# Kernel tuning notes

Measured on AMD Instinct MI355X. Metric: run time of the kernel, lower is better.

The kernel has to match this reference:

```python
import jax, jax.numpy as jnp
import numpy as np

N_E = 8192
E_DIM = 256
N_TOK = 32768
MU = 0.25  # commitment weight; beta=0 so diversity loss is skipped


def setup_inputs() -> dict:
    key = jax.random.key(0)
    k1, k2, k3 = jax.random.split(key, 3)
    x = jax.random.normal(k1, (N_TOK, E_DIM), dtype=jnp.float32)
    # codebook init: uniform(-1/n_e, 1/n_e) as in the torch module
    emb = jax.random.uniform(k2, (N_E, E_DIM), dtype=jnp.float32,
                             minval=-1.0 / N_E, maxval=1.0 / N_E)
    label = jax.random.randint(k3, (N_TOK,), 0, 10, dtype=jnp.int32)
    return {"x": x, "emb": emb, "label": label, "idx": 0}


def reference(x, emb, label, idx):
    # latent: [N, e_dim]
    latent = x.reshape(-1, emb.shape[1])
    # pairwise squared distances via norm + matmul: [N, n_e]
    d = (jnp.sum(latent * latent, axis=1, keepdims=True)
         + jnp.sum(emb * emb, axis=1)[None, :]
         - 2.0 * (latent @ emb.T))
    indices = jnp.argmin(d, axis=-1)                 # [N]
    x_q = emb[indices].reshape(x.shape)              # gather
    commitment_loss = jnp.mean(jnp.square(jax.lax.stop_gradient(x_q) - x))
    codebook_loss = jnp.mean(jnp.square(x_q - jax.lax.stop_gradient(x)))
    loss = codebook_loss + MU * commitment_loss      # beta=0 -> no diversity term
    x_q_out = x + jax.lax.stop_gradient(x_q - x)     # straight-through estimator
    return x_q_out, loss, indices.reshape(x.shape[:-1])
```

## Files before the change

### kernel.cpp

```cpp
#include <hip/hip_runtime.h>
#include <float.h>
#include <stdint.h>

#define N_TOK 32768
#define N_E   8192
#define EDIM  256
#define MU_W  0.25f
#define NSPLIT 4
#define NRANGE 2048
#define BMr 64
#define MARGIN_F 4096.0f
#define OFFSETF (-0x1p21f)
#define XSCALE 512.0f
#define ESCALE -131072.0f

typedef _Float16 f16;
typedef _Float16 f16x8 __attribute__((ext_vector_type(8)));
typedef _Float16 f16x4 __attribute__((ext_vector_type(4)));
typedef float f32x4 __attribute__((ext_vector_type(4)));
typedef unsigned int u32;
typedef unsigned long long u64;

#define WS_EMB16   0
#define WS_SX      4194304
#define WS_SE      4325376
#define WS_SE25    4358144
#define WS_CAND    4390912
#define WS_PART    6488064
#define WS_RCNT    6619136
#define WS_RLIST   6619392
#define WS_RBEST   6750464

__device__ inline void gload_lds16(const void* g, void* l) {
  __builtin_amdgcn_global_load_lds(
      (const __attribute__((address_space(1))) unsigned int*)g,
      (__attribute__((address_space(3))) unsigned int*)l, 16, 0, 0);
}

__device__ inline u32 umax_(u32 a, u32 b) { return a > b ? a : b; }
__device__ inline u32 umin_(u32 a, u32 b) { return a < b ? a : b; }

__device__ inline u32 med3u(u32 a, u32 b, u32 c) {
  u32 r;
  asm("v_med3_u32 %0, %1, %2, %3" : "=v"(r) : "v"(a), "v"(b), "v"(c));
  return r;
}

__device__ inline void ins4max(u32 v, u32& a, u32& b, u32& c, u32& d) {
  u32 na = umax_(a, v);
  u32 nb = med3u(a, b, v);
  u32 nc = med3u(b, c, v);
  u32 nd = med3u(c, d, v);
  a = na; b = nb; c = nc; d = nd;
}

__global__ __launch_bounds__(256) void conv_fused(const float* __restrict__ emb,
                                                  const float* __restrict__ x,
                                                  char* __restrict__ dst16,
                                                  float* __restrict__ se,
                                                  float* __restrict__ se25,
                                                  float* __restrict__ sx,
                                                  u32* __restrict__ rcnt) {
  if (blockIdx.x == 0 && threadIdx.x == 0) rcnt[0] = 0u;
  int wave = threadIdx.x >> 6;
  int lane = threadIdx.x & 63;
  int row = blockIdx.x * 4 + wave;
  if (row < N_E) {
    const float4 v = *(const float4*)(emb + (size_t)row * EDIM + lane * 4);
    float s = (v.x * v.x + v.y * v.y) + (v.z * v.z + v.w * v.w);
#pragma unroll
    for (int off = 32; off >= 1; off >>= 1) s += __shfl_xor(s, off);
    if (lane == 0) { se[row] = s; se25[row] = s * 0x1p25f; }
    f16x4 h;
    h[0] = (f16)(v.x * ESCALE); h[1] = (f16)(v.y * ESCALE);
    h[2] = (f16)(v.z * ESCALE); h[3] = (f16)(v.w * ESCALE);
    *(f16x4*)(dst16 + (size_t)(row >> 4) * 8192 + (lane >> 1) * 256 +
              (row & 15) * 16 + (lane & 1) * 8) = h;
  } else {
    int xr = row - N_E;
    const float4 v = *(const float4*)(x + (size_t)xr * EDIM + lane * 4);
    float s = (v.x * v.x + v.y * v.y) + (v.z * v.z + v.w * v.w);
#pragma unroll
    for (int off = 32; off >= 1; off >>= 1) s += __shfl_xor(s, off);
    if (lane == 0) sx[xr] = s;
  }
}

__global__ __launch_bounds__(256, 2) void vq_main(const float* __restrict__ x,
                                                  const char* __restrict__ e16,
                                                  const float* __restrict__ se25,
                                                  u32* __restrict__ cand) {
  __shared__ __align__(16) char lds[81920];
  char* Abuf = lds;
  char* Bbuf = lds + 32768;

  const int tid = threadIdx.x;
  const int lane = tid & 63;
  const int wn = tid >> 6;
  const int l15 = lane & 15;
  const int lg  = lane >> 4;
  const int split = blockIdx.x & 3;
  const int bm = (blockIdx.x >> 2) * BMr;
  const int nbase = split * NRANGE;
  const int splitRB = split * 128;

  int aOff[4], bOff[4];
#pragma unroll
  for (int mi = 0; mi < 4; ++mi) aOff[mi] = mi * 8192 + lg * 256 + l15 * 16;
#pragma unroll
  for (int ni = 0; ni < 4; ++ni) bOff[ni] = (wn * 4 + ni) * 1024 + lg * 256 + l15 * 16;

  int svo[4], sdo[4];
#pragma unroll
  for (int l = 0; l < 4; ++l) {
    int u = l * 256 + tid;
    svo[l] = (u >> 6) * 8192 + (u & 63) * 16;
    sdo[l] = (u >> 6) * 1024 + (u & 63) * 16;
  }

  {
    const int row = tid >> 2, seg = tid & 3;
    const float4* xs = (const float4*)(x + (size_t)(bm + row) * EDIM + seg * 64);
    const int ab = (row >> 4) * 8192 + (row & 15) * 16;
#pragma unroll
    for (int u = 0; u < 8; ++u) {
      float4 a0 = xs[2 * u], a1 = xs[2 * u + 1];
      f16x8 hv;
      hv[0] = (f16)(a0.x * XSCALE); hv[1] = (f16)(a0.y * XSCALE);
      hv[2] = (f16)(a0.z * XSCALE); hv[3] = (f16)(a0.w * XSCALE);
      hv[4] = (f16)(a1.x * XSCALE); hv[5] = (f16)(a1.y * XSCALE);
      hv[6] = (f16)(a1.z * XSCALE); hv[7] = (f16)(a1.w * XSCALE);
      *(f16x8*)&Abuf[ab + (seg * 8 + u) * 256] = hv;
    }
  }
  {
    const size_t eb = (size_t)splitRB * 8192;
#pragma unroll
    for (int l = 0; l < 4; ++l) gload_lds16(e16 + eb + svo[l], Bbuf + sdo[l]);
  }
  __syncthreads();

  u32 d1[16], d2[16], d3[16], d4[16];
#pragma unroll
  for (int s = 0; s < 16; ++s) { d1[s] = 0u; d2[s] = 0u; d3[s] = 0u; d4[s] = 0u; }

  const int idl = wn * 64 + l15;

  int bufc = 0;
  for (int t = 0; t < 8; ++t) {
    float sev[4];
#pragma unroll
    for (int ni = 0; ni < 4; ++ni)
      sev[ni] = se25[nbase + t * 256 + wn * 64 + ni * 16 + l15];

    f32x4 acc[4][4];
#pragma unroll
    for (int mi = 0; mi < 4; ++mi)
#pragma unroll
      for (int ni = 0; ni < 4; ++ni)
        acc[mi][ni] = (f32x4){OFFSETF, OFFSETF, OFFSETF, OFFSETF};

#pragma unroll
    for (int q = 0; q < 8; ++q) {
      const int c = t * 8 + q;
      const int cn = (c + 1) & 63;
      const int tn = cn >> 3, qn = cn & 7;
      const int bufn = (bufc == 2) ? 0 : bufc + 1;
      {
        const size_t ebN = (size_t)(splitRB + tn * 16) * 8192 + qn * 1024;
        char* dstN = Bbuf + bufn * 16384;
#pragma unroll
        for (int l = 0; l < 4; ++l) gload_lds16(e16 + ebN + svo[l], dstN + sdo[l]);
      }
      asm volatile("s_waitcnt vmcnt(4)" ::: "memory");
      __builtin_amdgcn_s_barrier();
      __builtin_amdgcn_sched_barrier(0);
      {
        const char* Bc = Bbuf + bufc * 16384;
        f16x8 av[4], bv[4];
#pragma unroll
        for (int mi = 0; mi < 4; ++mi) av[mi] = *(const f16x8*)&Abuf[aOff[mi] + q * 1024];
#pragma unroll
        for (int ni = 0; ni < 4; ++ni) bv[ni] = *(const f16x8*)&Bc[bOff[ni]];
        __builtin_amdgcn_s_setprio(1);
#pragma unroll
        for (int mi = 0; mi < 4; ++mi)
#pragma unroll
          for (int ni = 0; ni < 4; ++ni)
            acc[mi][ni] = __builtin_amdgcn_mfma_f32_16x16x32_f16(av[mi], bv[ni], acc[mi][ni], 0, 0, 0);
        __builtin_amdgcn_s_setprio(0);
      }
      bufc = bufn;
    }

#pragma unroll
    for (int ni = 0; ni < 4; ++ni) {
      const u32 id = (u32)(t * 256 + ni * 16 + idl);
#pragma unroll
      for (int mi = 0; mi < 4; ++mi)
#pragma unroll
        for (int r = 0; r < 4; ++r) {
          u32 up = (__float_as_uint(acc[mi][ni][r] + sev[ni]) & 0xFFFFF800u) | id;
          int s = mi * 4 + r;
          ins4max(up, d1[s], d2[s], d3[s], d4[s]);
        }
    }
  }

  __syncthreads();

#pragma unroll
  for (int off = 8; off >= 1; off >>= 1) {
#pragma unroll
    for (int s = 0; s < 16; ++s) {
      u32 e1 = (u32)__shfl_xor((int)d1[s], off);
      u32 e2 = (u32)__shfl_xor((int)d2[s], off);
      u32 e3 = (u32)__shfl_xor((int)d3[s], off);
      u32 e4 = (u32)__shfl_xor((int)d4[s], off);
      ins4max(e1, d1[s], d2[s], d3[s], d4[s]);
      ins4max(e2, d1[s], d2[s], d3[s], d4[s]);
      ins4max(e3, d1[s], d2[s], d3[s], d4[s]);
      ins4max(e4, d1[s], d2[s], d3[s], d4[s]);
    }
  }
  u32 (*scratch)[4][16][4] = (u32 (*)[4][16][4])lds;
  if (l15 == 0) {
#pragma unroll
    for (int s = 0; s < 16; ++s) {
      scratch[wn][lg][s][0] = d1[s];
      scratch[wn][lg][s][1] = d2[s];
      scratch[wn][lg][s][2] = d3[s];
      scratch[wn][lg][s][3] = d4[s];
    }
  }
  __syncthreads();
  if (tid < 64) {
    const int row = tid;
    const int mi = row >> 4, lgr = (row >> 2) & 3, rr = row & 3;
    const int s = mi * 4 + rr;
    u32 a1 = scratch[0][lgr][s][0];
    u32 a2 = scratch[0][lgr][s][1];
    u32 a3 = scratch[0][lgr][s][2];
    u32 a4 = scratch[0][lgr][s][3];
#pragma unroll
    for (int w = 1; w < 4; ++w) {
#pragma unroll
      for (int c = 0; c < 4; ++c)
        ins4max(scratch[w][lgr][s][c], a1, a2, a3, a4);
    }
    size_t base = (size_t)split * (N_TOK * 4) + (size_t)(bm + row) * 4;
    cand[base + 0] = a1; cand[base + 1] = a2; cand[base + 2] = a3; cand[base + 3] = a4;
  }
}

__global__ __launch_bounds__(256) void vq_gather_kernel(
    const float* __restrict__ x, const float* __restrict__ emb,
    const float* __restrict__ sx, const float* __restrict__ se,
    const u32* __restrict__ cand,
    float* __restrict__ out_q, float* __restrict__ out_idx,
    float* __restrict__ partials,
    u32* __restrict__ rcnt, u32* __restrict__ rlist, u64* __restrict__ rbest) {
  const int token = blockIdx.x;
  const int tid = threadIdx.x;
  __shared__ int s_j;
  __shared__ int s_cnt;
  __shared__ int s_cj[16];
  __shared__ float s_dv[16];
  __shared__ float red[4];

  if (tid == 0) {
    u32 u[16];
    float uf[16];
    float gmin = FLT_MAX;
#pragma unroll
    for (int sp = 0; sp < 4; ++sp)
#pragma unroll
      for (int c = 0; c < 4; ++c) {
        u32 v = cand[(size_t)sp * (N_TOK * 4) + (size_t)token * 4 + c];
        u[sp * 4 + c] = v;
        float f = __uint_as_float(v);
        uf[sp * 4 + c] = f;
        gmin = fminf(gmin, f);
      }
    bool guard = false;
#pragma unroll
    for (int sp = 0; sp < 4; ++sp) guard = guard || (uf[sp * 4 + 3] <= gmin + MARGIN_F);
    int cnt;
    if (guard) {
      u32 slot = atomicAdd(rcnt, 1u);
      rlist[slot] = (u32)token;
      rbest[slot] = ~0ull;
      cnt = -1;
    } else {
      cnt = 0;
#pragma unroll
      for (int sp = 0; sp < 4; ++sp)
#pragma unroll
        for (int c = 0; c < 4; ++c) {
          int k = sp * 4 + c;
          if (uf[k] <= gmin + MARGIN_F)
            s_cj[cnt++] = sp * NRANGE + (int)(u[k] & 0x7FFu);
        }
      if (cnt == 1) s_j = s_cj[0];
    }
    s_cnt = cnt;
  }
  __syncthreads();
  int cnt = s_cnt;
  if (cnt < 0) return;
  if (cnt > 1 && tid < cnt) {
    int j = s_cj[tid];
    const float* xr = x + (size_t)token * EDIM;
    const float* er = emb + (size_t)j * EDIM;
    float a = 0.f;
    for (int k = 0; k < EDIM; ++k) a = fmaf(xr[k], er[k], a);
    s_dv[tid] = (sx[token] + se[j]) - 2.0f * a;
  }
  __syncthreads();
  if (cnt > 1 && tid == 0) {
    float bd = s_dv[0]; int bj = s_cj[0];
    for (int c = 1; c < cnt; ++c) {
      float d = s_dv[c]; int j = s_cj[c];
      if (d < bd || (d == bd && j < bj)) { bd = d; bj = j; }
    }
    s_j = bj;
  }
  __syncthreads();
  const int j = s_j;
  if (tid == 0) out_idx[token] = (float)j;
  float xv = x[(size_t)token * EDIM + tid];
  float q  = emb[(size_t)j * EDIM + tid];
  float diff = q - xv;
  out_q[(size_t)token * EDIM + tid] = xv + diff;
  float sq = diff * diff;
#pragma unroll
  for (int off = 32; off >= 1; off >>= 1) sq += __shfl_xor(sq, off);
  const int wave = tid >> 6, lane = tid & 63;
  if (lane == 0) red[wave] = sq;
  __syncthreads();
  if (tid == 0) partials[token] = (red[0] + red[1]) + (red[2] + red[3]);
}

__global__ __launch_bounds__(256) void vq_rescan_scan(
    const float* __restrict__ x, const float* __restrict__ emb,
    const float* __restrict__ sx, const float* __restrict__ se,
    const u32* __restrict__ rcnt, const u32* __restrict__ rlist,
    u64* __restrict__ rbest) {
  const int tid = threadIdx.x;
  const int n = (int)rcnt[0];
  const int total = n * 32;
  __shared__ float xs[EDIM];
  __shared__ u64 rw[4];

  for (int w = blockIdx.x; w < total; w += gridDim.x) {
    const int it = w >> 5, chunk = w & 31;
    const int token = (int)rlist[it];
    __syncthreads();
    xs[tid] = x[(size_t)token * EDIM + tid];
    __syncthreads();
    const float sxt = sx[token];
    const int j = chunk * 256 + tid;
    const float* er = emb + (size_t)j * EDIM;
    float a = 0.f;
#pragma unroll 8
    for (int k4 = 0; k4 < 64; ++k4) {
      float4 e4 = ((const float4*)er)[k4];
      float4 x4 = ((const float4*)xs)[k4];
      a = fmaf(x4.x, e4.x, a);
      a = fmaf(x4.y, e4.y, a);
      a = fmaf(x4.z, e4.z, a);
      a = fmaf(x4.w, e4.w, a);
    }
    float d = (sxt + se[j]) - 2.0f * a;
    u64 pk = ((u64)__float_as_uint(d) << 32) | (u32)j;
    const int lane = tid & 63, wave = tid >> 6;
#pragma unroll
    for (int off = 32; off >= 1; off >>= 1) {
      u64 o = __shfl_xor(pk, off);
      pk = o < pk ? o : pk;
    }
    if (lane == 0) rw[wave] = pk;
    __syncthreads();
    if (tid == 0) {
      u64 b = rw[0];
#pragma unroll
      for (int ww = 1; ww < 4; ++ww) b = rw[ww] < b ? rw[ww] : b;
      atomicMin(rbest + it, b);
    }
  }
}

__global__ __launch_bounds__(256) void vq_rescan_write(
    const float* __restrict__ x, const float* __restrict__ emb,
    const u32* __restrict__ rcnt, const u32* __restrict__ rlist,
    const u64* __restrict__ rbest,
    float* __restrict__ out_q, float* __restrict__ out_idx,
    float* __restrict__ partials) {
  const int tid = threadIdx.x;
  const int n = (int)rcnt[0];
  __shared__ float red[4];

  for (int it = blockIdx.x; it < n; it += gridDim.x) {
    const int token = (int)rlist[it];
    const int j = (int)(u32)(rbest[it] & 0xFFFFFFFFull);
    if (tid == 0) out_idx[token] = (float)j;
    float xv = x[(size_t)token * EDIM + tid];
    float q  = emb[(size_t)j * EDIM + tid];
    float diff = q - xv;
    out_q[(size_t)token * EDIM + tid] = xv + diff;
    float sq = diff * diff;
#pragma unroll
    for (int off = 32; off >= 1; off >>= 1) sq += __shfl_xor(sq, off);
    const int lane = tid & 63, wave = tid >> 6;
    __syncthreads();
    if (lane == 0) red[wave] = sq;
    __syncthreads();
    if (tid == 0) partials[token] = (red[0] + red[1]) + (red[2] + red[3]);
  }
}

__global__ __launch_bounds__(256) void vq_loss_kernel(const float* __restrict__ partials,
                                                      float* __restrict__ loss_out) {
  const int tid = threadIdx.x;
  float s = 0.f;
  for (int i = tid; i < N_TOK; i += 256) s += partials[i];
  __shared__ float red[4];
#pragma unroll
  for (int off = 32; off >= 1; off >>= 1) s += __shfl_xor(s, off);
  const int wave = tid >> 6, lane = tid & 63;
  if (lane == 0) red[wave] = s;
  __syncthreads();
  if (tid == 0) {
    float tot = (red[0] + red[1]) + (red[2] + red[3]);
    float mean = tot / (float)(N_TOK * EDIM);
    loss_out[0] = mean + MU_W * mean;
  }
}

extern "C" void kernel_launch(void* const* d_in, const int* in_sizes, int n_in,
                              void* d_out, int out_size, void* d_ws, size_t ws_size,
                              hipStream_t stream) {
  const float* x   = (const float*)d_in[0];
  const float* emb = (const float*)d_in[1];

  float* out      = (float*)d_out;
  float* out_q    = out;
  float* out_loss = out + (size_t)N_TOK * EDIM;
  float* out_idx  = out_loss + 1;

  char* w = (char*)d_ws;
  char*  emb16    = w + WS_EMB16;
  float* sx       = (float*)(w + WS_SX);
  float* se       = (float*)(w + WS_SE);
  float* se25     = (float*)(w + WS_SE25);
  u32*   cand     = (u32*)(w + WS_CAND);
  float* partials = (float*)(w + WS_PART);
  u32*   rcnt     = (u32*)(w + WS_RCNT);
  u32*   rlist    = (u32*)(w + WS_RLIST);
  u64*   rbest    = (u64*)(w + WS_RBEST);

  conv_fused<<<(N_E + N_TOK) / 4, 256, 0, stream>>>(emb, x, emb16, se, se25, sx, rcnt);

  vq_main<<<NSPLIT * (N_TOK / BMr), 256, 0, stream>>>(x, emb16, se25, cand);

  vq_gather_kernel<<<N_TOK, 256, 0, stream>>>(x, emb, sx, se, cand, out_q, out_idx, partials,
                                              rcnt, rlist, rbest);
  vq_rescan_scan<<<2048, 256, 0, stream>>>(x, emb, sx, se, rcnt, rlist, rbest);
  vq_rescan_write<<<64, 256, 0, stream>>>(x, emb, rcnt, rlist, rbest, out_q, out_idx, partials);
  vq_loss_kernel<<<1, 256, 0, stream>>>(partials, out_loss);
}
```

Before: 314.8 us.

## Switch candidate search GEMM from fp16 to int8 MFMA with 8-way codebook split

Result: slower. 968.6 us (+207.7%).

```diff
diff --git a/kernel.cpp b/kernel.cpp
--- a/kernel.cpp
+++ b/kernel.cpp
@@ -6,26 +6,21 @@
 #define N_E   8192
 #define EDIM  256
 #define MU_W  0.25f
-#define NSPLIT 4
-#define NRANGE 2048
+#define NSPLIT 8
+#define NRANGE 1024
 #define BMr 64
-#define MARGIN_F 4096.0f
-#define OFFSETF (-0x1p21f)
-#define XSCALE 512.0f
-#define ESCALE -131072.0f
-
-typedef _Float16 f16;
-typedef _Float16 f16x8 __attribute__((ext_vector_type(8)));
-typedef _Float16 f16x4 __attribute__((ext_vector_type(4)));
-typedef float f32x4 __attribute__((ext_vector_type(4)));
+#define MARGIN_I 6144u
+#define SEVB_BIAS (1 << 20)
+
+typedef int i32x4 __attribute__((ext_vector_type(4)));
 typedef unsigned int u32;
 typedef unsigned long long u64;
 
-#define WS_EMB16   0
-#define WS_SX      4194304
-#define WS_SE      4325376
-#define WS_SE25    4358144
-#define WS_CAND    4390912
+#define WS_E8      0
+#define WS_SX      2097152
+#define WS_SE      2228224
+#define WS_SEVB    2260992
+#define WS_CAND    2293760
 #define WS_PART    6488064
 #define WS_RCNT    6619136
 #define WS_RLIST   6619392
@@ -37,7 +32,6 @@
       (__attribute__((address_space(3))) unsigned int*)l, 16, 0, 0);
 }
 
-__device__ inline u32 umax_(u32 a, u32 b) { return a > b ? a : b; }
 __device__ inline u32 umin_(u32 a, u32 b) { return a < b ? a : b; }
 
 __device__ inline u32 med3u(u32 a, u32 b, u32 c) {
@@ -46,19 +40,21 @@
   return r;
 }
 
-__device__ inline void ins4max(u32 v, u32& a, u32& b, u32& c, u32& d) {
-  u32 na = umax_(a, v);
+__device__ inline void ins4min(u32 v, u32& a, u32& b, u32& c, u32& d) {
+  u32 na = umin_(a, v);
   u32 nb = med3u(a, b, v);
   u32 nc = med3u(b, c, v);
   u32 nd = med3u(c, d, v);
   a = na; b = nb; c = nc; d = nd;
 }
 
+__device__ inline int clamp127(int q) { return q < -127 ? -127 : (q > 127 ? 127 : q); }
+
 __global__ __launch_bounds__(256) void conv_fused(const float* __restrict__ emb,
                                                   const float* __restrict__ x,
-                                                  char* __restrict__ dst16,
+                                                  char* __restrict__ e8,
                                                   float* __restrict__ se,
-                                                  float* __restrict__ se25,
+                                                  int* __restrict__ sevb,
                                                   float* __restrict__ sx,
                                                   u32* __restrict__ rcnt) {
   if (blockIdx.x == 0 && threadIdx.x == 0) rcnt[0] = 0u;
@@ -70,12 +66,19 @@
     float s = (v.x * v.x + v.y * v.y) + (v.z * v.z + v.w * v.w);
 #pragma unroll
     for (int off = 32; off >= 1; off >>= 1) s += __shfl_xor(s, off);
-    if (lane == 0) { se[row] = s; se25[row] = s * 0x1p25f; }
-    f16x4 h;
-    h[0] = (f16)(v.x * ESCALE); h[1] = (f16)(v.y * ESCALE);
-    h[2] = (f16)(v.z * ESCALE); h[3] = (f16)(v.w * ESCALE);
-    *(f16x4*)(dst16 + (size_t)(row >> 4) * 8192 + (lane >> 1) * 256 +
-              (row & 15) * 16 + (lane & 1) * 8) = h;
+    if (lane == 0) se[row] = s;
+    int q0 = (int)rintf(v.x * 524288.f);
+    int q1 = (int)rintf(v.y * 524288.f);
+    int q2 = (int)rintf(v.z * 524288.f);
+    int q3 = (int)rintf(v.w * 524288.f);
+    int s2 = q0 * q0 + q1 * q1 + q2 * q2 + q3 * q3;
+#pragma unroll
+    for (int off = 32; off >= 1; off >>= 1) s2 += __shfl_xor(s2, off);
+    if (lane == 0) sevb[row] = ((s2 + 16384) >> 15) + SEVB_BIAS;
+    u32 w = (u32)(q0 & 255) | ((u32)(q1 & 255) << 8) |
+            ((u32)(q2 & 255) << 16) | ((u32)(q3 & 255) << 24);
+    *(u32*)(e8 + (size_t)(row >> 4) * 4096 + (lane >> 2) * 256 +
+            (row & 15) * 16 + (lane & 3) * 4) = w;
   } else {
     int xr = row - N_E;
     const float4 v = *(const float4*)(x + (size_t)xr * EDIM + lane * 4);
@@ -87,26 +90,25 @@
 }
 
 __global__ __launch_bounds__(256, 2) void vq_main(const float* __restrict__ x,
-                                                  const char* __restrict__ e16,
-                                                  const float* __restrict__ se25,
+                                                  const char* __restrict__ e8,
+                                                  const int* __restrict__ sevb,
                                                   u32* __restrict__ cand) {
-  __shared__ __align__(16) char lds[81920];
-  char* Abuf = lds;
-  char* Bbuf = lds + 32768;
+  __shared__ __align__(16) char lds[65536];
+  char* Bbuf = lds + 16384;
 
   const int tid = threadIdx.x;
   const int lane = tid & 63;
   const int wn = tid >> 6;
   const int l15 = lane & 15;
   const int lg  = lane >> 4;
-  const int split = blockIdx.x & 3;
-  const int bm = (blockIdx.x >> 2) * BMr;
+  const int split = blockIdx.x & 7;
+  const int bm = (blockIdx.x >> 3) * BMr;
   const int nbase = split * NRANGE;
-  const int splitRB = split * 128;
+  const int splitRB = split * 64;
 
   int aOff[4], bOff[4];
 #pragma unroll
-  for (int mi = 0; mi < 4; ++mi) aOff[mi] = mi * 8192 + lg * 256 + l15 * 16;
+  for (int mi = 0; mi < 4; ++mi) aOff[mi] = mi * 4096 + lg * 256 + l15 * 16;
 #pragma unroll
   for (int ni = 0; ni < 4; ++ni) bOff[ni] = (wn * 4 + ni) * 1024 + lg * 256 + l15 * 16;
 
@@ -114,95 +116,101 @@
 #pragma unroll
   for (int l = 0; l < 4; ++l) {
     int u = l * 256 + tid;
-    svo[l] = (u >> 6) * 8192 + (u & 63) * 16;
-    sdo[l] = (u >> 6) * 1024 + (u & 63) * 16;
-  }
+    svo[l] = (u >> 6) * 4096 + (u & 63) * 16;
+    sdo[l] = u * 16;
+  }
+
+  int sv[4][4];
+#pragma unroll
+  for (int ct = 0; ct < 4; ++ct)
+#pragma unroll
+    for (int ni = 0; ni < 4; ++ni)
+      sv[ct][ni] = sevb[nbase + ct * 256 + wn * 64 + ni * 16 + l15];
 
   {
     const int row = tid >> 2, seg = tid & 3;
     const float4* xs = (const float4*)(x + (size_t)(bm + row) * EDIM + seg * 64);
-    const int ab = (row >> 4) * 8192 + (row & 15) * 16;
-#pragma unroll
-    for (int u = 0; u < 8; ++u) {
-      float4 a0 = xs[2 * u], a1 = xs[2 * u + 1];
-      f16x8 hv;
-      hv[0] = (f16)(a0.x * XSCALE); hv[1] = (f16)(a0.y * XSCALE);
-      hv[2] = (f16)(a0.z * XSCALE); hv[3] = (f16)(a0.w * XSCALE);
-      hv[4] = (f16)(a1.x * XSCALE); hv[5] = (f16)(a1.y * XSCALE);
-      hv[6] = (f16)(a1.z * XSCALE); hv[7] = (f16)(a1.w * XSCALE);
-      *(f16x8*)&Abuf[ab + (seg * 8 + u) * 256] = hv;
-    }
-  }
-  {
-    const size_t eb = (size_t)splitRB * 8192;
-#pragma unroll
-    for (int l = 0; l < 4; ++l) gload_lds16(e16 + eb + svo[l], Bbuf + sdo[l]);
-  }
-  __syncthreads();
+    char* ab = lds + (row >> 4) * 4096 + (row & 15) * 16;
+#pragma unroll
+    for (int u = 0; u < 4; ++u) {
+      u32 w[4];
+#pragma unroll
+      for (int p = 0; p < 4; ++p) {
+        float4 f = xs[u * 4 + p];
+        int q0 = clamp127((int)rintf(f.x * 16.f));
+        int q1 = clamp127((int)rintf(f.y * 16.f));
+        int q2 = clamp127((int)rintf(f.z * 16.f));
+        int q3 = clamp127((int)rintf(f.w * 16.f));
+        w[p] = (u32)(q0 & 255) | ((u32)(q1 & 255) << 8) |
+               ((u32)(q2 & 255) << 16) | ((u32)(q3 & 255) << 24);
+      }
+      *(uint4*)(ab + (seg * 4 + u) * 256) = make_uint4(w[0], w[1], w[2], w[3]);
+    }
+  }
+  __syncthreads();
+
+#pragma unroll
+  for (int c0 = 0; c0 < 2; ++c0) {
+    const char* src = e8 + (size_t)(splitRB + (c0 >> 2) * 16) * 4096 + (c0 & 3) * 1024;
+    char* dst = Bbuf + (c0 % 3) * 16384;
+#pragma unroll
+    for (int l = 0; l < 4; ++l) gload_lds16(src + svo[l], dst + sdo[l]);
+  }
 
   u32 d1[16], d2[16], d3[16], d4[16];
 #pragma unroll
-  for (int s = 0; s < 16; ++s) { d1[s] = 0u; d2[s] = 0u; d3[s] = 0u; d4[s] = 0u; }
+  for (int s = 0; s < 16; ++s) { d1[s] = 0xFFFFFFFFu; d2[s] = 0xFFFFFFFFu; d3[s] = 0xFFFFFFFFu; d4[s] = 0xFFFFFFFFu; }
 
   const int idl = wn * 64 + l15;
 
-  int bufc = 0;
-  for (int t = 0; t < 8; ++t) {
-    float sev[4];
-#pragma unroll
-    for (int ni = 0; ni < 4; ++ni)
-      sev[ni] = se25[nbase + t * 256 + wn * 64 + ni * 16 + l15];
-
-    f32x4 acc[4][4];
+#pragma unroll
+  for (int ct = 0; ct < 4; ++ct) {
+    i32x4 acc[4][4];
 #pragma unroll
     for (int mi = 0; mi < 4; ++mi)
 #pragma unroll
-      for (int ni = 0; ni < 4; ++ni)
-        acc[mi][ni] = (f32x4){OFFSETF, OFFSETF, OFFSETF, OFFSETF};
-
-#pragma unroll
-    for (int q = 0; q < 8; ++q) {
-      const int c = t * 8 + q;
-      const int cn = (c + 1) & 63;
-      const int tn = cn >> 3, qn = cn & 7;
-      const int bufn = (bufc == 2) ? 0 : bufc + 1;
-      {
-        const size_t ebN = (size_t)(splitRB + tn * 16) * 8192 + qn * 1024;
-        char* dstN = Bbuf + bufn * 16384;
-#pragma unroll
-        for (int l = 0; l < 4; ++l) gload_lds16(e16 + ebN + svo[l], dstN + sdo[l]);
-      }
+      for (int ni = 0; ni < 4; ++ni) acc[mi][ni] = (i32x4){0, 0, 0, 0};
+
+#pragma unroll
+    for (int q = 0; q < 4; ++q) {
+      const int c = ct * 4 + q;
       asm volatile("s_waitcnt vmcnt(4)" ::: "memory");
       __builtin_amdgcn_s_barrier();
       __builtin_amdgcn_sched_barrier(0);
       {
-        const char* Bc = Bbuf + bufc * 16384;
-        f16x8 av[4], bv[4];
-#pragma unroll
-        for (int mi = 0; mi < 4; ++mi) av[mi] = *(const f16x8*)&Abuf[aOff[mi] + q * 1024];
-#pragma unroll
-        for (int ni = 0; ni < 4; ++ni) bv[ni] = *(const f16x8*)&Bc[bOff[ni]];
-        __builtin_amdgcn_s_setprio(1);
-#pragma unroll
-        for (int mi = 0; mi < 4; ++mi)
-#pragma unroll
-          for (int ni = 0; ni < 4; ++ni)
-            acc[mi][ni] = __builtin_amdgcn_mfma_f32_16x16x32_f16(av[mi], bv[ni], acc[mi][ni], 0, 0, 0);
-        __builtin_amdgcn_s_setprio(0);
+        const int cn = (c + 2) & 15;
+        const char* src = e8 + (size_t)(splitRB + (cn >> 2) * 16) * 4096 + (cn & 3) * 1024;
+        char* dst = Bbuf + ((c + 2) % 3) * 16384;
+#pragma unroll
+        for (int l = 0; l < 4; ++l) gload_lds16(src + svo[l], dst + sdo[l]);
       }
-      bufc = bufn;
+      const int rb = (c % 3) * 16384;
+      i32x4 av[4], bv[4];
+#pragma unroll
+      for (int mi = 0; mi < 4; ++mi) av[mi] = *(const i32x4*)&lds[aOff[mi] + q * 1024];
+#pragma unroll
+      for (int ni = 0; ni < 4; ++ni) bv[ni] = *(const i32x4*)&Bbuf[rb + bOff[ni]];
+      __builtin_amdgcn_s_setprio(1);
+#pragma unroll
+      for (int mi = 0; mi < 4; ++mi)
+#pragma unroll
+        for (int ni = 0; ni < 4; ++ni)
+          acc[mi][ni] = __builtin_amdgcn_mfma_i32_16x16x64_i8(av[mi], bv[ni], acc[mi][ni], 0, 0, 0);
+      __builtin_amdgcn_s_setprio(0);
     }
 
 #pragma unroll
     for (int ni = 0; ni < 4; ++ni) {
-      const u32 id = (u32)(t * 256 + ni * 16 + idl);
+      const u32 id = (u32)(ct * 256 + ni * 16 + idl);
+      const int svn = sv[ct][ni];
 #pragma unroll
       for (int mi = 0; mi < 4; ++mi)
 #pragma unroll
         for (int r = 0; r < 4; ++r) {
-          u32 up = (__float_as_uint(acc[mi][ni][r] + sev[ni]) & 0xFFFFF800u) | id;
+          int dot = acc[mi][ni][r];
+          u32 up = ((u32)(svn - dot - dot) << 11) | id;
           int s = mi * 4 + r;
-          ins4max(up, d1[s], d2[s], d3[s], d4[s]);
+          ins4min(up, d1[s], d2[s], d3[s], d4[s]);
         }
     }
   }
@@ -217,10 +225,10 @@
       u32 e2 = (u32)__shfl_xor((int)d2[s], off);
       u32 e3 = (u32)__shfl_xor((int)d3[s], off);
       u32 e4 = (u32)__shfl_xor((int)d4[s], off);
-      ins4max(e1, d1[s], d2[s], d3[s], d4[s]);
-      ins4max(e2, d1[s], d2[s], d3[s], d4[s]);
-      ins4max(e3, d1[s], d2[s], d3[s], d4[s]);
-      ins4max(e4, d1[s], d2[s], d3[s], d4[s]);
+      ins4min(e1, d1[s], d2[s], d3[s], d4[s]);
+      ins4min(e2, d1[s], d2[s], d3[s], d4[s]);
+      ins4min(e3, d1[s], d2[s], d3[s], d4[s]);
+      ins4min(e4, d1[s], d2[s], d3[s], d4[s]);
     }
   }
   u32 (*scratch)[4][16][4] = (u32 (*)[4][16][4])lds;
@@ -246,7 +254,7 @@
     for (int w = 1; w < 4; ++w) {
 #pragma unroll
       for (int c = 0; c < 4; ++c)
-        ins4max(scratch[w][lgr][s][c], a1, a2, a3, a4);
+        ins4min(scratch[w][lgr][s][c], a1, a2, a3, a4);
     }
     size_t base = (size_t)split * (N_TOK * 4) + (size_t)(bm + row) * 4;
     cand[base + 0] = a1; cand[base + 1] = a2; cand[base + 2] = a3; cand[base + 3] = a4;
@@ -264,27 +272,25 @@
   const int tid = threadIdx.x;
   __shared__ int s_j;
   __shared__ int s_cnt;
-  __shared__ int s_cj[16];
-  __shared__ float s_dv[16];
+  __shared__ int s_cj[32];
+  __shared__ float s_dv[32];
   __shared__ float red[4];
 
   if (tid == 0) {
-    u32 u[16];
-    float uf[16];
-    float gmin = FLT_MAX;
-#pragma unroll
-    for (int sp = 0; sp < 4; ++sp)
+    u32 u_[32];
+    u32 sbmin = 0xFFFFFFFFu;
+#pragma unroll
+    for (int sp = 0; sp < 8; ++sp)
 #pragma unroll
       for (int c = 0; c < 4; ++c) {
         u32 v = cand[(size_t)sp * (N_TOK * 4) + (size_t)token * 4 + c];
-        u[sp * 4 + c] = v;
-        float f = __uint_as_float(v);
-        uf[sp * 4 + c] = f;
-        gmin = fminf(gmin, f);
+        u_[sp * 4 + c] = v;
+        sbmin = umin_(sbmin, v >> 11);
       }
+    const u32 thr = sbmin + MARGIN_I;
     bool guard = false;
 #pragma unroll
-    for (int sp = 0; sp < 4; ++sp) guard = guard || (uf[sp * 4 + 3] <= gmin + MARGIN_F);
+    for (int sp = 0; sp < 8; ++sp) guard = guard || ((u_[sp * 4 + 3] >> 11) <= thr);
     int cnt;
     if (guard) {
       u32 slot = atomicAdd(rcnt, 1u);
@@ -294,12 +300,12 @@
     } else {
       cnt = 0;
 #pragma unroll
-      for (int sp = 0; sp < 4; ++sp)
+      for (int sp = 0; sp < 8; ++sp)
 #pragma unroll
         for (int c = 0; c < 4; ++c) {
-          int k = sp * 4 + c;
-          if (uf[k] <= gmin + MARGIN_F)
-            s_cj[cnt++] = sp * NRANGE + (int)(u[k] & 0x7FFu);
+          u32 v = u_[sp * 4 + c];
+          if ((v >> 11) <= thr)
+            s_cj[cnt++] = sp * NRANGE + (int)(v & 0x7FFu);
         }
       if (cnt == 1) s_j = s_cj[0];
     }
@@ -449,19 +455,19 @@
   float* out_idx  = out_loss + 1;
 
   char* w = (char*)d_ws;
-  char*  emb16    = w + WS_EMB16;
+  char*  e8       = w + WS_E8;
   float* sx       = (float*)(w + WS_SX);
   float* se       = (float*)(w + WS_SE);
-  float* se25     = (float*)(w + WS_SE25);
+  int*   sevb     = (int*)(w + WS_SEVB);
   u32*   cand     = (u32*)(w + WS_CAND);
   float* partials = (float*)(w + WS_PART);
   u32*   rcnt     = (u32*)(w + WS_RCNT);
   u32*   rlist    = (u32*)(w + WS_RLIST);
   u64*   rbest    = (u64*)(w + WS_RBEST);
 
-  conv_fused<<<(N_E + N_TOK) / 4, 256, 0, stream>>>(emb, x, emb16, se, se25, sx, rcnt);
-
-  vq_main<<<NSPLIT * (N_TOK / BMr), 256, 0, stream>>>(x, emb16, se25, cand);
+  conv_fused<<<(N_E + N_TOK) / 4, 256, 0, stream>>>(emb, x, e8, se, sevb, sx, rcnt);
+
+  vq_main<<<NSPLIT * (N_TOK / BMr), 256, 0, stream>>>(x, e8, sevb, cand);
 
   vq_gather_kernel<<<N_TOK, 256, 0, stream>>>(x, emb, sx, se, cand, out_q, out_idx, partials,
                                               rcnt, rlist, rbest);
```

## Load codebook fragments directly from global into registers, drop LDS B staging

Applied to the files above, without the earlier changes.

After: 683.9 us. +117.3%, slower.

```diff
diff --git a/kernel.cpp b/kernel.cpp
--- a/kernel.cpp
+++ b/kernel.cpp
@@ -30,12 +30,6 @@
 #define WS_RCNT    6619136
 #define WS_RLIST   6619392
 #define WS_RBEST   6750464
-
-__device__ inline void gload_lds16(const void* g, void* l) {
-  __builtin_amdgcn_global_load_lds(
-      (const __attribute__((address_space(1))) unsigned int*)g,
-      (__attribute__((address_space(3))) unsigned int*)l, 16, 0, 0);
-}
 
 __device__ inline u32 umax_(u32 a, u32 b) { return a > b ? a : b; }
 __device__ inline u32 umin_(u32 a, u32 b) { return a < b ? a : b; }
@@ -86,13 +80,11 @@
   }
 }
 
-__global__ __launch_bounds__(256, 2) void vq_main(const float* __restrict__ x,
+__global__ __launch_bounds__(256, 3) void vq_main(const float* __restrict__ x,
                                                   const char* __restrict__ e16,
                                                   const float* __restrict__ se25,
                                                   u32* __restrict__ cand) {
-  __shared__ __align__(16) char lds[81920];
-  char* Abuf = lds;
-  char* Bbuf = lds + 32768;
+  __shared__ __align__(16) char Abuf[32768];
 
   const int tid = threadIdx.x;
   const int lane = tid & 63;
@@ -102,21 +94,10 @@
   const int split = blockIdx.x & 3;
   const int bm = (blockIdx.x >> 2) * BMr;
   const int nbase = split * NRANGE;
-  const int splitRB = split * 128;
-
-  int aOff[4], bOff[4];
+
+  int aOff[4];
 #pragma unroll
   for (int mi = 0; mi < 4; ++mi) aOff[mi] = mi * 8192 + lg * 256 + l15 * 16;
-#pragma unroll
-  for (int ni = 0; ni < 4; ++ni) bOff[ni] = (wn * 4 + ni) * 1024 + lg * 256 + l15 * 16;
-
-  int svo[4], sdo[4];
-#pragma unroll
-  for (int l = 0; l < 4; ++l) {
-    int u = l * 256 + tid;
-    svo[l] = (u >> 6) * 8192 + (u & 63) * 16;
-    sdo[l] = (u >> 6) * 1024 + (u & 63) * 16;
-  }
 
   {
     const int row = tid >> 2, seg = tid & 3;
@@ -133,12 +114,14 @@
       *(f16x8*)&Abuf[ab + (seg * 8 + u) * 256] = hv;
     }
   }
-  {
-    const size_t eb = (size_t)splitRB * 8192;
-#pragma unroll
-    for (int l = 0; l < 4; ++l) gload_lds16(e16 + eb + svo[l], Bbuf + sdo[l]);
-  }
-  __syncthreads();
+  __syncthreads();
+
+  const char* ebase = e16 + (size_t)(split * 128 + wn * 4) * 8192 + lg * 256 + l15 * 16;
+
+  f16x8 bvA[4], bvB[4];
+#pragma unroll
+  for (int ni = 0; ni < 4; ++ni)
+    bvA[ni] = *(const f16x8*)(ebase + (size_t)ni * 8192);
 
   u32 d1[16], d2[16], d3[16], d4[16];
 #pragma unroll
@@ -146,7 +129,6 @@
 
   const int idl = wn * 64 + l15;
 
-  int bufc = 0;
   for (int t = 0; t < 8; ++t) {
     float sev[4];
 #pragma unroll
@@ -162,35 +144,33 @@
 
 #pragma unroll
     for (int q = 0; q < 8; ++q) {
-      const int c = t * 8 + q;
-      const int cn = (c + 1) & 63;
-      const int tn = cn >> 3, qn = cn & 7;
-      const int bufn = (bufc == 2) ? 0 : bufc + 1;
-      {
-        const size_t ebN = (size_t)(splitRB + tn * 16) * 8192 + qn * 1024;
-        char* dstN = Bbuf + bufn * 16384;
-#pragma unroll
-        for (int l = 0; l < 4; ++l) gload_lds16(e16 + ebN + svo[l], dstN + sdo[l]);
-      }
-      asm volatile("s_waitcnt vmcnt(4)" ::: "memory");
-      __builtin_amdgcn_s_barrier();
-      __builtin_amdgcn_sched_barrier(0);
-      {
-        const char* Bc = Bbuf + bufc * 16384;
-        f16x8 av[4], bv[4];
-#pragma unroll
-        for (int mi = 0; mi < 4; ++mi) av[mi] = *(const f16x8*)&Abuf[aOff[mi] + q * 1024];
-#pragma unroll
-        for (int ni = 0; ni < 4; ++ni) bv[ni] = *(const f16x8*)&Bc[bOff[ni]];
+      const int c1 = (t * 8 + q + 1) & 63;
+      const int ntt = c1 >> 3, nq = c1 & 7;
+      const char* src = ebase + (size_t)(ntt * 16) * 8192 + nq * 1024;
+      f16x8 av[4];
+#pragma unroll
+      for (int mi = 0; mi < 4; ++mi) av[mi] = *(const f16x8*)&Abuf[aOff[mi] + q * 1024];
+      if ((q & 1) == 0) {
+#pragma unroll
+        for (int ni = 0; ni < 4; ++ni) bvB[ni] = *(const f16x8*)(src + (size_t)ni * 8192);
         __builtin_amdgcn_s_setprio(1);
 #pragma unroll
         for (int mi = 0; mi < 4; ++mi)
 #pragma unroll
           for (int ni = 0; ni < 4; ++ni)
-            acc[mi][ni] = __builtin_amdgcn_mfma_f32_16x16x32_f16(av[mi], bv[ni], acc[mi][ni], 0, 0, 0);
+            acc[mi][ni] = __builtin_amdgcn_mfma_f32_16x16x32_f16(av[mi], bvA[ni], acc[mi][ni], 0, 0, 0);
+        __builtin_amdgcn_s_setprio(0);
+      } else {
+#pragma unroll
+        for (int ni = 0; ni < 4; ++ni) bvA[ni] = *(const f16x8*)(src + (size_t)ni * 8192);
+        __builtin_amdgcn_s_setprio(1);
+#pragma unroll
+        for (int mi = 0; mi < 4; ++mi)
+#pragma unroll
+          for (int ni = 0; ni < 4; ++ni)
+            acc[mi][ni] = __builtin_amdgcn_mfma_f32_16x16x32_f16(av[mi], bvB[ni], acc[mi][ni], 0, 0, 0);
         __builtin_amdgcn_s_setprio(0);
       }
-      bufc = bufn;
     }
 
 #pragma unroll
@@ -206,8 +186,6 @@
         }
     }
   }
-
-  __syncthreads();
 
 #pragma unroll
   for (int off = 8; off >= 1; off >>= 1) {
@@ -223,7 +201,8 @@
       ins4max(e4, d1[s], d2[s], d3[s], d4[s]);
     }
   }
-  u32 (*scratch)[4][16][4] = (u32 (*)[4][16][4])lds;
+  __syncthreads();
+  u32 (*scratch)[4][16][4] = (u32 (*)[4][16][4])Abuf;
   if (l15 == 0) {
 #pragma unroll
     for (int s = 0; s < 16; ++s) {
@@ -269,7 +248,7 @@
   __shared__ float red[4];
 
   if (tid == 0) {
-    u32 u[16];
+    u32 u_[16];
     float uf[16];
     float gmin = FLT_MAX;
 #pragma unroll
@@ -277,7 +256,7 @@
 #pragma unroll
       for (int c = 0; c < 4; ++c) {
         u32 v = cand[(size_t)sp * (N_TOK * 4) + (size_t)token * 4 + c];
-        u[sp * 4 + c] = v;
+        u_[sp * 4 + c] = v;
         float f = __uint_as_float(v);
         uf[sp * 4 + c] = f;
         gmin = fminf(gmin, f);
@@ -299,7 +278,7 @@
         for (int c = 0; c < 4; ++c) {
           int k = sp * 4 + c;
           if (uf[k] <= gmin + MARGIN_F)
-            s_cj[cnt++] = sp * NRANGE + (int)(u[k] & 0x7FFu);
+            s_cj[cnt++] = sp * NRANGE + (int)(u_[k] & 0x7FFu);
         }
       if (cnt == 1) s_j = s_cj[0];
     }
```
